# Kernel tuning notes

Measured on AMD Instinct MI355X. Metric: run time of the kernel, lower is better.

## Reference

```python
import jax, jax.numpy as jnp
import numpy as np

B, NTILES, FSZ, R = 16, 16384, 2048, 5


def setup_inputs() -> dict:
    key = jax.random.key(0)
    ks = jax.random.split(key, 8)
    feats = jax.random.normal(ks[0], (B, NTILES, FSZ), dtype=jnp.float32)
    # conv1x1: Conv1d(2048, 1, kernel_size=1, bias=False) -> weight [1, 2048, 1] == vector [2048]
    w_conv = jax.random.normal(ks[1], (FSZ,), dtype=jnp.float32) * 0.02
    # MLP: Linear(10,200) -> Sigmoid -> Dropout -> Linear(200,100) -> Sigmoid -> Dropout -> Linear(100,1)
    W1 = jax.random.normal(ks[2], (200, 2 * R), dtype=jnp.float32) * 0.1
    b1 = jnp.zeros((200,), dtype=jnp.float32)
    W2 = jax.random.normal(ks[3], (100, 200), dtype=jnp.float32) * 0.1
    b2 = jnp.zeros((100,), dtype=jnp.float32)
    W3 = jax.random.normal(ks[4], (1, 100), dtype=jnp.float32) * 0.1
    b3 = jnp.zeros((1,), dtype=jnp.float32)
    return {"feats": feats, "w_conv": w_conv, "W1": W1, "b1": b1,
            "W2": W2, "b2": b2, "W3": W3, "b3": b3}


def reference(feats, w_conv, W1, b1, W2, b2, W3, b3):
    # 1x1 conv over channel dim == per-tile dot product with w_conv -> scores [B, ntiles]
    scores = jnp.einsum('bnf,f->bn', feats, w_conv)
    # full sort, then bottom-R and top-R scores (torch: sort + gather on min/max indices)
    vals = jnp.sort(scores, axis=1)
    minmax = jnp.concatenate([vals[:, :R], vals[:, -R:]], axis=1)  # [B, 2R]
    # tiny MLP (eval mode: dropout = identity)
    h = jax.nn.sigmoid(minmax @ W1.T + b1)
    h = jax.nn.sigmoid(h @ W2.T + b2)
    logits = h @ W3.T + b3  # [B, 1]
    probs = jax.nn.sigmoid(logits)
    return logits, probs
```

## Files before the change

### kernel.cpp

```cpp
#include <hip/hip_runtime.h>
#include <math.h>

#define FSZ 2048
#define NTILES 16384
#define BATCH 16
#define RSEL 5

__global__ __launch_bounds__(256) void score_kernel(
    const float* __restrict__ feats,
    const float* __restrict__ w_conv,
    float* __restrict__ scores,
    int total_tiles)
{
    __shared__ float4 wsh[FSZ / 4];
    const float4* w4 = reinterpret_cast<const float4*>(w_conv);
    for (int i = threadIdx.x; i < FSZ / 4; i += blockDim.x) wsh[i] = w4[i];
    __syncthreads();

    const int lane          = threadIdx.x & 63;
    const int wave          = threadIdx.x >> 6;
    const int wavesPerBlock = blockDim.x >> 6;
    const int globalWave    = blockIdx.x * wavesPerBlock + wave;
    const int totalWaves    = gridDim.x * wavesPerBlock;

    for (int tile = globalWave; tile < total_tiles; tile += totalWaves) {
        const float4* f4 = reinterpret_cast<const float4*>(feats + (size_t)tile * FSZ);
        float acc = 0.f;
#pragma unroll
        for (int k = 0; k < 8; ++k) {
            float4 a = f4[lane + 64 * k];
            float4 w = wsh[lane + 64 * k];
            acc += a.x * w.x + a.y * w.y + a.z * w.z + a.w * w.w;
        }
#pragma unroll
        for (int off = 32; off > 0; off >>= 1)
            acc += __shfl_xor(acc, off, 64);
        if (lane == 0) scores[tile] = acc;
    }
}

__global__ __launch_bounds__(256) void select_kernel(
    const float* __restrict__ scores,
    float* __restrict__ minmax)
{
    const int b   = blockIdx.x;
    const int tid = threadIdx.x;
    const float* s = scores + b * NTILES;

    float mn[RSEL], mx[RSEL];
#pragma unroll
    for (int i = 0; i < RSEL; ++i) { mn[i] = INFINITY; mx[i] = -INFINITY; }

    for (int t = tid; t < NTILES; t += 256) {
        float v = s[t];
        if (v < mn[RSEL - 1]) {
            mn[RSEL - 1] = v;
#pragma unroll
            for (int i = RSEL - 1; i > 0; --i)
                if (mn[i] < mn[i - 1]) { float tmp = mn[i]; mn[i] = mn[i - 1]; mn[i - 1] = tmp; }
        }
        if (v > mx[RSEL - 1]) {
            mx[RSEL - 1] = v;
#pragma unroll
            for (int i = RSEL - 1; i > 0; --i)
                if (mx[i] > mx[i - 1]) { float tmp = mx[i]; mx[i] = mx[i - 1]; mx[i - 1] = tmp; }
        }
    }

    __shared__ float smn[256][RSEL];
    __shared__ float smx[256][RSEL];
#pragma unroll
    for (int i = 0; i < RSEL; ++i) { smn[tid][i] = mn[i]; smx[tid][i] = mx[i]; }

    for (int stride = 128; stride > 0; stride >>= 1) {
        __syncthreads();
        if (tid < stride) {
            float amn[RSEL], bmn[RSEL], omn[RSEL];
            float amx[RSEL], bmx[RSEL], omx[RSEL];
#pragma unroll
            for (int i = 0; i < RSEL; ++i) {
                amn[i] = smn[tid][i];  bmn[i] = smn[tid + stride][i];
                amx[i] = smx[tid][i];  bmx[i] = smx[tid + stride][i];
            }
            int ia = 0, ib = 0;
#pragma unroll
            for (int i = 0; i < RSEL; ++i)
                omn[i] = (amn[ia] <= bmn[ib]) ? amn[ia++] : bmn[ib++];
            ia = 0; ib = 0;
#pragma unroll
            for (int i = 0; i < RSEL; ++i)
                omx[i] = (amx[ia] >= bmx[ib]) ? amx[ia++] : bmx[ib++];
#pragma unroll
            for (int i = 0; i < RSEL; ++i) { smn[tid][i] = omn[i]; smx[tid][i] = omx[i]; }
        }
    }
    __syncthreads();
    if (tid == 0) {
#pragma unroll
        for (int i = 0; i < RSEL; ++i) {
            minmax[b * 2 * RSEL + i]        = smn[0][i];
            minmax[b * 2 * RSEL + RSEL + i] = smx[0][RSEL - 1 - i];
        }
    }
}

__global__ __launch_bounds__(256) void mlp_kernel(
    const float* __restrict__ minmax,
    const float* __restrict__ W1, const float* __restrict__ b1,
    const float* __restrict__ W2, const float* __restrict__ b2,
    const float* __restrict__ W3, const float* __restrict__ b3,
    float* __restrict__ out)
{
    const int b   = blockIdx.x;
    const int tid = threadIdx.x;
    __shared__ float x[2 * RSEL];
    __shared__ float h1[200];
    __shared__ float h2[100];

    if (tid < 2 * RSEL) x[tid] = minmax[b * 2 * RSEL + tid];
    __syncthreads();

    if (tid < 200) {
        float acc = b1[tid];
#pragma unroll
        for (int i = 0; i < 2 * RSEL; ++i) acc += W1[tid * 2 * RSEL + i] * x[i];
        h1[tid] = 1.f / (1.f + expf(-acc));
    }
    __syncthreads();

    if (tid < 100) {
        float acc = b2[tid];
        for (int i = 0; i < 200; ++i) acc += W2[tid * 200 + i] * h1[i];
        h2[tid] = 1.f / (1.f + expf(-acc));
    }
    __syncthreads();

    if (tid == 0) {
        float acc = b3[0];
        for (int i = 0; i < 100; ++i) acc += W3[i] * h2[i];
        out[b]         = acc;
        out[BATCH + b] = 1.f / (1.f + expf(-acc));
    }
}

extern "C" void kernel_launch(void* const* d_in, const int* in_sizes, int n_in,
                              void* d_out, int out_size, void* d_ws, size_t ws_size,
                              hipStream_t stream)
{
    const float* feats  = (const float*)d_in[0];
    const float* w_conv = (const float*)d_in[1];
    const float* W1     = (const float*)d_in[2];
    const float* b1     = (const float*)d_in[3];
    const float* W2     = (const float*)d_in[4];
    const float* b2     = (const float*)d_in[5];
    const float* W3     = (const float*)d_in[6];
    const float* b3     = (const float*)d_in[7];
    float* out = (float*)d_out;

    float* scores = (float*)d_ws;
    float* minmax = scores + (size_t)BATCH * NTILES;

    const int total_tiles = BATCH * NTILES;
    score_kernel<<<2048, 256, 0, stream>>>(feats, w_conv, scores, total_tiles);
    select_kernel<<<BATCH, 256, 0, stream>>>(scores, minmax);
    mlp_kernel<<<BATCH, 256, 0, stream>>>(minmax, W1, b1, W2, b2, W3, b3, out);
}
```

Baseline: 417.0 us.

## Keep conv weights in registers, process two tiles per wave, fuse select and MLP

The score kernel now loads the conv weight slice into registers instead of shared memory and has each wave process two tiles per iteration using nontemporal vector loads, which puts more loads in flight on the bandwidth-bound 2 GiB feature read. The select kernel reads scores as float4 and is fused with the MLP kernel, removing one launch and the minmax round trip through global memory. The cost is higher register pressure, and the nontemporal hint may change cache behaviour.

```diff
diff --git a/kernel.cpp b/kernel.cpp
--- a/kernel.cpp
+++ b/kernel.cpp
@@ -6,64 +6,83 @@
 #define BATCH 16
 #define RSEL 5
 
+typedef float f32x4 __attribute__((ext_vector_type(4)));
+
 __global__ __launch_bounds__(256) void score_kernel(
     const float* __restrict__ feats,
     const float* __restrict__ w_conv,
     float* __restrict__ scores,
     int total_tiles)
 {
-    __shared__ float4 wsh[FSZ / 4];
-    const float4* w4 = reinterpret_cast<const float4*>(w_conv);
-    for (int i = threadIdx.x; i < FSZ / 4; i += blockDim.x) wsh[i] = w4[i];
-    __syncthreads();
+    const int lane       = threadIdx.x & 63;
+    const int wave       = threadIdx.x >> 6;
+    const int globalWave = blockIdx.x * 4 + wave;
+    const int totalWaves = gridDim.x * 4;
 
-    const int lane          = threadIdx.x & 63;
-    const int wave          = threadIdx.x >> 6;
-    const int wavesPerBlock = blockDim.x >> 6;
-    const int globalWave    = blockIdx.x * wavesPerBlock + wave;
-    const int totalWaves    = gridDim.x * wavesPerBlock;
+    const f32x4* w4 = reinterpret_cast<const f32x4*>(w_conv);
+    f32x4 wreg[8];
+#pragma unroll
+    for (int k = 0; k < 8; ++k) wreg[k] = w4[lane + 64 * k];
 
-    for (int tile = globalWave; tile < total_tiles; tile += totalWaves) {
-        const float4* f4 = reinterpret_cast<const float4*>(feats + (size_t)tile * FSZ);
-        float acc = 0.f;
+    for (int t = globalWave * 2; t < total_tiles; t += 2 * totalWaves) {
+        const f32x4* fa = reinterpret_cast<const f32x4*>(feats + (size_t)t * FSZ);
+        const f32x4* fb = fa + FSZ / 4;
+
+        float acca = 0.f, accb = 0.f;
 #pragma unroll
         for (int k = 0; k < 8; ++k) {
-            float4 a = f4[lane + 64 * k];
-            float4 w = wsh[lane + 64 * k];
-            acc += a.x * w.x + a.y * w.y + a.z * w.z + a.w * w.w;
+            f32x4 a = __builtin_nontemporal_load(fa + lane + 64 * k);
+            acca += a.x * wreg[k].x + a.y * wreg[k].y + a.z * wreg[k].z + a.w * wreg[k].w;
         }
 #pragma unroll
-        for (int off = 32; off > 0; off >>= 1)
-            acc += __shfl_xor(acc, off, 64);
-        if (lane == 0) scores[tile] = acc;
+        for (int k = 0; k < 8; ++k) {
+            f32x4 b = __builtin_nontemporal_load(fb + lane + 64 * k);
+            accb += b.x * wreg[k].x + b.y * wreg[k].y + b.z * wreg[k].z + b.w * wreg[k].w;
+        }
+#pragma unroll
+        for (int off = 32; off > 0; off >>= 1) {
+            acca += __shfl_xor(acca, off, 64);
+            accb += __shfl_xor(accb, off, 64);
+        }
+        if (lane == 0) {
+            scores[t]     = acca;
+            scores[t + 1] = accb;
+        }
     }
 }
 
-__global__ __launch_bounds__(256) void select_kernel(
+__global__ __launch_bounds__(256) void select_mlp_kernel(
     const float* __restrict__ scores,
-    float* __restrict__ minmax)
+    const float* __restrict__ W1, const float* __restrict__ b1,
+    const float* __restrict__ W2, const float* __restrict__ b2,
+    const float* __restrict__ W3, const float* __restrict__ b3,
+    float* __restrict__ out)
 {
     const int b   = blockIdx.x;
     const int tid = threadIdx.x;
-    const float* s = scores + b * NTILES;
+    const f32x4* s4 = reinterpret_cast<const f32x4*>(scores + b * NTILES);
 
     float mn[RSEL], mx[RSEL];
 #pragma unroll
     for (int i = 0; i < RSEL; ++i) { mn[i] = INFINITY; mx[i] = -INFINITY; }
 
-    for (int t = tid; t < NTILES; t += 256) {
-        float v = s[t];
-        if (v < mn[RSEL - 1]) {
-            mn[RSEL - 1] = v;
+    for (int t = tid; t < NTILES / 4; t += 256) {
+        f32x4 v4 = s4[t];
 #pragma unroll
-            for (int i = RSEL - 1; i > 0; --i)
-                if (mn[i] < mn[i - 1]) { float tmp = mn[i]; mn[i] = mn[i - 1]; mn[i - 1] = tmp; }
-        }
-        if (v > mx[RSEL - 1]) {
-            mx[RSEL - 1] = v;
+        for (int j = 0; j < 4; ++j) {
+            float v = v4[j];
+            if (v < mn[RSEL - 1]) {
+                mn[RSEL - 1] = v;
 #pragma unroll
-            for (int i = RSEL - 1; i > 0; --i)
-                if (mx[i] > mx[i - 1]) { float tmp = mx[i]; mx[i] = mx[i - 1]; mx[i - 1] = tmp; }
+                for (int i = RSEL - 1; i > 0; --i)
+                    if (mn[i] < mn[i - 1]) { float tmp = mn[i]; mn[i] = mn[i - 1]; mn[i - 1] = tmp; }
+            }
+            if (v > mx[RSEL - 1]) {
+                mx[RSEL - 1] = v;
+#pragma unroll
+                for (int i = RSEL - 1; i > 0; --i)
+                    if (mx[i] > mx[i - 1]) { float tmp = mx[i]; mx[i] = mx[i - 1]; mx[i - 1] = tmp; }
+            }
         }
     }
 
@@ -95,29 +114,12 @@
         }
     }
     __syncthreads();
-    if (tid == 0) {
-#pragma unroll
-        for (int i = 0; i < RSEL; ++i) {
-            minmax[b * 2 * RSEL + i]        = smn[0][i];
-            minmax[b * 2 * RSEL + RSEL + i] = smx[0][RSEL - 1 - i];
-        }
-    }
-}
 
-__global__ __launch_bounds__(256) void mlp_kernel(
-    const float* __restrict__ minmax,
-    const float* __restrict__ W1, const float* __restrict__ b1,
-    const float* __restrict__ W2, const float* __restrict__ b2,
-    const float* __restrict__ W3, const float* __restrict__ b3,
-    float* __restrict__ out)
-{
-    const int b   = blockIdx.x;
-    const int tid = threadIdx.x;
     __shared__ float x[2 * RSEL];
     __shared__ float h1[200];
     __shared__ float h2[100];
-
-    if (tid < 2 * RSEL) x[tid] = minmax[b * 2 * RSEL + tid];
+    if (tid < RSEL)                       x[tid] = smn[0][tid];
+    else if (tid < 2 * RSEL)              x[tid] = smx[0][2 * RSEL - 1 - tid];
     __syncthreads();
 
     if (tid < 200) {
@@ -158,10 +160,8 @@
     float* out = (float*)d_out;
 
     float* scores = (float*)d_ws;
-    float* minmax = scores + (size_t)BATCH * NTILES;
 
     const int total_tiles = BATCH * NTILES;
     score_kernel<<<2048, 256, 0, stream>>>(feats, w_conv, scores, total_tiles);
-    select_kernel<<<BATCH, 256, 0, stream>>>(scores, minmax);
-    mlp_kernel<<<BATCH, 256, 0, stream>>>(minmax, W1, b1, W2, b2, W3, b3, out);
+    select_mlp_kernel<<<BATCH, 256, 0, stream>>>(scores, W1, b1, W2, b2, W3, b3, out);
 }
```

Result: faster. 358.8 us (-14.0%).
